# Optimization experiments

Measured on AMD Instinct MI355X. Metric: run time of the kernel, lower is better.

Reference implementation:

```python
import jax, jax.numpy as jnp
import numpy as np

N_NODES = 100000
N_EDGES = 1600000
IN_F, HID, OUT_F = 256, 128, 64
GAMMA = 1.0

def _glorot(key, shape):
    lim = (6.0 / (shape[0] + shape[1])) ** 0.5
    return jax.random.uniform(key, shape, jnp.float32, -lim, lim)

def setup_inputs() -> dict:
    key = jax.random.key(0)
    ks = jax.random.split(key, 8)
    x = jax.random.normal(ks[0], (N_NODES, IN_F), jnp.float32)
    src = jax.random.randint(ks[1], (N_EDGES,), 0, N_NODES)
    dst = jax.random.randint(ks[2], (N_EDGES,), 0, N_NODES)
    return dict(
        x=x, src=src, dst=dst,
        w_mean1=_glorot(ks[3], (IN_F, HID)), w_var1=_glorot(ks[4], (IN_F, HID)),
        b_mean1=jnp.zeros((HID,), jnp.float32), b_var1=jnp.zeros((HID,), jnp.float32),
        w_mean2=_glorot(ks[5], (HID, OUT_F)), w_var2=_glorot(ks[6], (HID, OUT_F)),
        b_mean2=jnp.zeros((OUT_F,), jnp.float32), b_var2=jnp.zeros((OUT_F,), jnp.float32),
    )

def _conv(mean_in, var_in, wm, wv, bm, bv, src, dst, norm1, norm2, gamma, act):
    n = norm1.shape[0]
    mean = jax.nn.relu(mean_in @ wm + bm)
    var = jax.nn.relu(var_in @ wv + bv)
    att = jnp.exp(-gamma * var)            # attention reweighting
    m = mean * att * norm1                  # pre-scaled messages [N, d]
    v = var * (att * att) * norm2
    # copy_u + sum: gather at src, scatter-add at dst
    mean = jax.ops.segment_sum(m[src], dst, num_segments=n) * norm1
    var = jax.ops.segment_sum(v[src], dst, num_segments=n) * norm2
    if act:
        mean, var = jax.nn.relu(mean), jax.nn.relu(var)
    return mean, var

def reference(x, src, dst, w_mean1, w_var1, b_mean1, b_var1,
              w_mean2, w_var2, b_mean2, b_var2):
    n = x.shape[0]
    ones = jnp.ones(dst.shape, jnp.float32)
    degs = jnp.clip(jax.ops.segment_sum(ones, dst, num_segments=n), 1.0, None)
    norm1 = (degs ** -0.5)[:, None]  # D^{-1/2}
    norm2 = norm1 * norm1            # D^{-1}
    # dropout is identity (eval mode) for a deterministic reference
    mean, var = _conv(x, x, w_mean1, w_var1, b_mean1, b_var1,
                      src, dst, norm1, norm2, GAMMA, True)
    mean, var = _conv(mean, var, w_mean2, w_var2, b_mean2, b_var2,
                      src, dst, norm1, norm2, GAMMA, False)
    std = jnp.sqrt(var + 1e-8)
    eps = jax.random.normal(jax.random.key(42), std.shape, std.dtype)
    return eps * std + mean
```

## Files before the change

kernel.cpp:

```cpp
#include <hip/hip_runtime.h>

#define GN 100000
#define GE 1600000

__device__ __forceinline__ unsigned bf16r(float f) {
  unsigned u = __float_as_uint(f);
  return (u + 0x7FFFu + ((u >> 16) & 1u)) >> 16;
}
__device__ __forceinline__ unsigned pack2(float lo, float hi) {
  return bf16r(lo) | (bf16r(hi) << 16);
}
__device__ __forceinline__ float bflo(unsigned u) { return __uint_as_float(u << 16); }
__device__ __forceinline__ float bfhi(unsigned u) { return __uint_as_float(u & 0xFFFF0000u); }

__device__ __forceinline__ unsigned rotl32(unsigned x, int r) { return (x << r) | (x >> (32 - r)); }

__device__ __forceinline__ void threefry2x32(unsigned k0, unsigned k1,
                                             unsigned c0, unsigned c1,
                                             unsigned& o0, unsigned& o1) {
  const unsigned ks2 = k0 ^ k1 ^ 0x1BD11BDAu;
  unsigned x0 = c0 + k0, x1 = c1 + k1;
#define TF_R4(ra, rb, rc, rd) \
  x0 += x1; x1 = rotl32(x1, ra); x1 ^= x0; \
  x0 += x1; x1 = rotl32(x1, rb); x1 ^= x0; \
  x0 += x1; x1 = rotl32(x1, rc); x1 ^= x0; \
  x0 += x1; x1 = rotl32(x1, rd); x1 ^= x0;
  TF_R4(13, 15, 26, 6)  x0 += k1;  x1 += ks2 + 1u;
  TF_R4(17, 29, 16, 24) x0 += ks2; x1 += k0 + 2u;
  TF_R4(13, 15, 26, 6)  x0 += k0;  x1 += k1 + 3u;
  TF_R4(17, 29, 16, 24) x0 += k1;  x1 += ks2 + 4u;
  TF_R4(13, 15, 26, 6)  x0 += ks2; x1 += k0 + 5u;
#undef TF_R4
  o0 = x0; o1 = x1;
}

__device__ __forceinline__ float bits_to_normal(unsigned bits) {
  const float lo = -0.99999994f;
  const float u = __uint_as_float((bits >> 9) | 0x3f800000u) - 1.0f;
  float x = u * 2.0f + lo;
  x = fmaxf(x, lo);
  float w = -log1pf(-x * x);
  float p;
  if (w < 5.0f) {
    w -= 2.5f;
    p = 2.81022636e-08f;
    p = fmaf(p, w, 3.43273939e-07f);
    p = fmaf(p, w, -3.5233877e-06f);
    p = fmaf(p, w, -4.39150654e-06f);
    p = fmaf(p, w, 0.00021858087f);
    p = fmaf(p, w, -0.00125372503f);
    p = fmaf(p, w, -0.00417768164f);
    p = fmaf(p, w, 0.246640727f);
    p = fmaf(p, w, 1.50140941f);
  } else {
    w = sqrtf(w) - 3.0f;
    p = -0.000200214257f;
    p = fmaf(p, w, 0.000100950558f);
    p = fmaf(p, w, 0.00134934322f);
    p = fmaf(p, w, -0.00367342844f);
    p = fmaf(p, w, 0.00573950773f);
    p = fmaf(p, w, -0.0076224613f);
    p = fmaf(p, w, 0.00943887047f);
    p = fmaf(p, w, 1.00167406f);
    p = fmaf(p, w, 2.83297682f);
  }
  return 1.41421356f * p * x;
}

__global__ void hist_kernel(const int* __restrict__ dst, int* __restrict__ hist) {
  const int e = blockIdx.x * 256 + threadIdx.x;
  if (e < GE) atomicAdd(&hist[dst[e]], 1);
}

__global__ __launch_bounds__(1024) void scan_kernel(const int* __restrict__ hist,
                                                    int* __restrict__ row_ptr) {
  __shared__ int wsum[16];
  __shared__ int carry_s;
  const int t = threadIdx.x, lane = t & 63, wave = t >> 6;
  if (t == 0) carry_s = 0;
  __syncthreads();
  for (int base = 0; base < GN; base += 4096) {
    const int idx = base + t * 4;
    const int h0 = (idx + 0 < GN) ? hist[idx + 0] : 0;
    const int h1 = (idx + 1 < GN) ? hist[idx + 1] : 0;
    const int h2 = (idx + 2 < GN) ? hist[idx + 2] : 0;
    const int h3 = (idx + 3 < GN) ? hist[idx + 3] : 0;
    const int p0 = h0, p1 = h0 + h1, p2 = h0 + h1 + h2, p3 = h0 + h1 + h2 + h3;
    int s = p3;
#pragma unroll
    for (int o = 1; o < 64; o <<= 1) {
      const int u = __shfl_up(s, o, 64);
      if (lane >= o) s += u;
    }
    if (lane == 63) wsum[wave] = s;
    __syncthreads();
    int woff = 0;
    for (int w2 = 0; w2 < wave; w2++) woff += wsum[w2];
    const int carry = carry_s;
    __syncthreads();
    const int tb = carry + woff + (s - p3);
    if (idx + 0 < GN) row_ptr[idx + 0] = tb;
    if (idx + 1 < GN) row_ptr[idx + 1] = tb + p0;
    if (idx + 2 < GN) row_ptr[idx + 2] = tb + p1;
    if (idx + 3 < GN) row_ptr[idx + 3] = tb + p2;
    if (t == 1023) carry_s = carry + woff + s;
    __syncthreads();
  }
  if (t == 0) row_ptr[GN] = carry_s;
}

__global__ void norm_kernel(const int* __restrict__ hist,
                            float* __restrict__ norm1, float* __restrict__ norm2) {
  const int i = blockIdx.x * 256 + threadIdx.x;
  if (i < GN) {
    const double d = (double)max(hist[i], 1);
    norm1[i] = (float)(1.0 / sqrt(d));
    norm2[i] = (float)(1.0 / d);
  }
}

__global__ void fill_kernel(const int* __restrict__ src, const int* __restrict__ dst,
                            const int* __restrict__ row_ptr, int* __restrict__ fillc,
                            int* __restrict__ csr) {
  const int e = blockIdx.x * 256 + threadIdx.x;
  if (e < GE) {
    const int d = dst[e];
    const int pos = atomicAdd(&fillc[d], 1);
    csr[row_ptr[d] + pos] = src[e];
  }
}

#define FMA8(acc, a, p0, p1)                                                        \
  acc[0] = fmaf(a, p0.x, acc[0]); acc[1] = fmaf(a, p0.y, acc[1]);                   \
  acc[2] = fmaf(a, p0.z, acc[2]); acc[3] = fmaf(a, p0.w, acc[3]);                   \
  acc[4] = fmaf(a, p1.x, acc[4]); acc[5] = fmaf(a, p1.y, acc[5]);                   \
  acc[6] = fmaf(a, p1.z, acc[6]); acc[7] = fmaf(a, p1.w, acc[7]);

__global__ __launch_bounds__(256) void gemm1_kernel(
    const float* __restrict__ x,
    const float* __restrict__ wm, const float* __restrict__ wv,
    const float* __restrict__ bm, const float* __restrict__ bv,
    const float* __restrict__ norm1, const float* __restrict__ norm2,
    unsigned* __restrict__ mv16) {
  __shared__ float xs[64][33];
  __shared__ float wms[32][128];
  __shared__ float wvs[32][128];
  const int t = threadIdx.x;
  const int row0 = blockIdx.x * 64;
  const int ty = t >> 4, tx = t & 15;
  float accm[4][8] = {};
  float accv[4][8] = {};
  for (int k0 = 0; k0 < 256; k0 += 32) {
#pragma unroll
    for (int i = 0; i < 2; i++) {
      const int f = t + (i << 8);
      const int r = f >> 3, c4 = (f & 7) << 2;
      const int rg = min(row0 + r, GN - 1);
      *(float4*)&xs[r][c4] = *(const float4*)&x[(size_t)rg * 256 + k0 + c4];
    }
#pragma unroll
    for (int i = 0; i < 4; i++) {
      const int f = t + (i << 8);
      const int kk = f >> 5, j4 = (f & 31) << 2;
      *(float4*)&wms[kk][j4] = *(const float4*)&wm[(size_t)(k0 + kk) * 128 + j4];
      *(float4*)&wvs[kk][j4] = *(const float4*)&wv[(size_t)(k0 + kk) * 128 + j4];
    }
    __syncthreads();
#pragma unroll 4
    for (int kk = 0; kk < 32; kk++) {
      const float4 bm0 = *(const float4*)&wms[kk][tx * 4];
      const float4 bm1 = *(const float4*)&wms[kk][tx * 4 + 64];
      const float4 bv0 = *(const float4*)&wvs[kk][tx * 4];
      const float4 bv1 = *(const float4*)&wvs[kk][tx * 4 + 64];
#pragma unroll
      for (int r = 0; r < 4; r++) {
        const float a = xs[ty * 4 + r][kk];
        FMA8(accm[r], a, bm0, bm1)
        FMA8(accv[r], a, bv0, bv1)
      }
    }
    __syncthreads();
  }
  float bmv[8], bvv[8];
#pragma unroll
  for (int j = 0; j < 4; j++) {
    bmv[j] = bm[tx * 4 + j];      bmv[4 + j] = bm[tx * 4 + 64 + j];
    bvv[j] = bv[tx * 4 + j];      bvv[4 + j] = bv[tx * 4 + 64 + j];
  }
#pragma unroll
  for (int rr = 0; rr < 4; rr++) {
    const int i = row0 + ty * 4 + rr;
    if (i >= GN) break;
    const float n1 = norm1[i], n2 = norm2[i];
    float om[8], ov[8];
#pragma unroll
    for (int j = 0; j < 8; j++) {
      const float mean = fmaxf(accm[rr][j] + bmv[j], 0.f);
      const float var  = fmaxf(accv[rr][j] + bvv[j], 0.f);
      const float att = expf(-var);
      om[j] = mean * att * n1;
      ov[j] = var * att * att * n2;
    }
    *(uint4*)(mv16 + (size_t)i * 128 + tx * 4) =
        make_uint4(pack2(om[0], om[1]), pack2(ov[0], ov[1]),
                   pack2(om[2], om[3]), pack2(ov[2], ov[3]));
    *(uint4*)(mv16 + (size_t)i * 128 + 64 + tx * 4) =
        make_uint4(pack2(om[4], om[5]), pack2(ov[4], ov[5]),
                   pack2(om[6], om[7]), pack2(ov[6], ov[7]));
  }
}

__global__ __launch_bounds__(256) void agg1_kernel(
    const int* __restrict__ row_ptr, const int* __restrict__ csr,
    const uint2* __restrict__ mv16,
    const float* __restrict__ norm1, const float* __restrict__ norm2,
    float* __restrict__ hmv) {
  const int wave = threadIdx.x >> 6, lane = threadIdx.x & 63;
  const int i = blockIdx.x * 4 + wave;
  const int e0 = row_ptr[i], e1 = row_ptr[i + 1];
  float amx0 = 0.f, amy0 = 0.f, avx0 = 0.f, avy0 = 0.f;
  float amx1 = 0.f, amy1 = 0.f, avx1 = 0.f, avy1 = 0.f;
  int e = e0;
  for (; e + 4 <= e1; e += 4) {
    const int s0 = csr[e], s1 = csr[e + 1], s2 = csr[e + 2], s3 = csr[e + 3];
    const uint2 q0 = mv16[(size_t)s0 * 64 + lane];
    const uint2 q1 = mv16[(size_t)s1 * 64 + lane];
    const uint2 q2 = mv16[(size_t)s2 * 64 + lane];
    const uint2 q3 = mv16[(size_t)s3 * 64 + lane];
    amx0 += bflo(q0.x) + bflo(q1.x); amx1 += bflo(q2.x) + bflo(q3.x);
    amy0 += bfhi(q0.x) + bfhi(q1.x); amy1 += bfhi(q2.x) + bfhi(q3.x);
    avx0 += bflo(q0.y) + bflo(q1.y); avx1 += bflo(q2.y) + bflo(q3.y);
    avy0 += bfhi(q0.y) + bfhi(q1.y); avy1 += bfhi(q2.y) + bfhi(q3.y);
  }
  for (; e < e1; e++) {
    const uint2 q0 = mv16[(size_t)csr[e] * 64 + lane];
    amx0 += bflo(q0.x); amy0 += bfhi(q0.x);
    avx0 += bflo(q0.y); avy0 += bfhi(q0.y);
  }
  const float amx = amx0 + amx1, amy = amy0 + amy1;
  const float avx = avx0 + avx1, avy = avy0 + avy1;
  const float n1 = norm1[i], n2 = norm2[i];
  float4 o;
  o.x = fmaxf(amx * n1, 0.f);
  o.y = fmaxf(avx * n2, 0.f);
  o.z = fmaxf(amy * n1, 0.f);
  o.w = fmaxf(avy * n2, 0.f);
  *(float4*)&hmv[(size_t)i * 256 + lane * 4] = o;
}

__global__ __launch_bounds__(256) void gemm2_kernel(
    const float* __restrict__ hmv,
    const float* __restrict__ wm2, const float* __restrict__ wv2,
    const float* __restrict__ bm2, const float* __restrict__ bv2,
    const float* __restrict__ norm1, const float* __restrict__ norm2,
    unsigned* __restrict__ m2v16) {
  __shared__ float wsh[2][64][64];
  const int t = threadIdx.x;
  const int r = t >> 3, c0 = (t & 7) << 3;
  const int i = blockIdx.x * 32 + r;
  const float* hrow = hmv + (size_t)i * 256;
  float accm[8] = {}, accv[8] = {};
  for (int kc = 0; kc < 2; kc++) {
#pragma unroll
    for (int ii = 0; ii < 4; ii++) {
      const int f4 = t + (ii << 8);
      const int k = f4 >> 4, j4 = (f4 & 15) << 2;
      *(float4*)&wsh[0][k][j4] = *(const float4*)&wm2[(size_t)(kc * 64 + k) * 64 + j4];
      *(float4*)&wsh[1][k][j4] = *(const float4*)&wv2[(size_t)(kc * 64 + k) * 64 + j4];
    }
    __syncthreads();
#pragma unroll 8
    for (int kk = 0; kk < 64; kk++) {
      const float2 hh = *(const float2*)&hrow[(kc * 64 + kk) * 2];
      const float4 b0 = *(const float4*)&wsh[0][kk][c0];
      const float4 b1 = *(const float4*)&wsh[0][kk][c0 + 4];
      const float4 d0 = *(const float4*)&wsh[1][kk][c0];
      const float4 d1 = *(const float4*)&wsh[1][kk][c0 + 4];
      FMA8(accm, hh.x, b0, b1)
      FMA8(accv, hh.y, d0, d1)
    }
    __syncthreads();
  }
  const float n1 = norm1[i], n2 = norm2[i];
  unsigned pk[8];
#pragma unroll
  for (int j = 0; j < 8; j++) {
    const float mean2 = fmaxf(accm[j] + bm2[c0 + j], 0.f);
    const float var2  = fmaxf(accv[j] + bv2[c0 + j], 0.f);
    const float att = expf(-var2);
    pk[j] = pack2(mean2 * att * n1, var2 * att * att * n2);
  }
  unsigned* dstp = m2v16 + (size_t)i * 64 + c0;
  *(uint4*)(dstp)     = make_uint4(pk[0], pk[1], pk[2], pk[3]);
  *(uint4*)(dstp + 4) = make_uint4(pk[4], pk[5], pk[6], pk[7]);
}

__global__ __launch_bounds__(256) void agg2_reparam_kernel(
    const int* __restrict__ row_ptr, const int* __restrict__ csr,
    const unsigned* __restrict__ m2v16,
    const float* __restrict__ norm1, const float* __restrict__ norm2,
    float* __restrict__ out) {
  const int wave = threadIdx.x >> 6, lane = threadIdx.x & 63;
  const int i = blockIdx.x * 4 + wave;
  const int e0 = row_ptr[i], e1 = row_ptr[i + 1];
  float am0 = 0.f, av0 = 0.f, am1 = 0.f, av1 = 0.f;
  int e = e0;
  for (; e + 4 <= e1; e += 4) {
    const int s0 = csr[e], s1 = csr[e + 1], s2 = csr[e + 2], s3 = csr[e + 3];
    const unsigned q0 = m2v16[(size_t)s0 * 64 + lane];
    const unsigned q1 = m2v16[(size_t)s1 * 64 + lane];
    const unsigned q2 = m2v16[(size_t)s2 * 64 + lane];
    const unsigned q3 = m2v16[(size_t)s3 * 64 + lane];
    am0 += bflo(q0) + bflo(q1); am1 += bflo(q2) + bflo(q3);
    av0 += bfhi(q0) + bfhi(q1); av1 += bfhi(q2) + bfhi(q3);
  }
  for (; e < e1; e++) {
    const unsigned q0 = m2v16[(size_t)csr[e] * 64 + lane];
    am0 += bflo(q0); av0 += bfhi(q0);
  }
  const float mean = (am0 + am1) * norm1[i];
  const float var  = (av0 + av1) * norm2[i];
  const int b = i * 64 + lane;
  unsigned o0, o1;
  threefry2x32(0u, 42u, 0u, (unsigned)b, o0, o1);
  const float eps = bits_to_normal(o0 ^ o1);
  out[b] = eps * sqrtf(var + 1e-8f) + mean;
}

extern "C" void kernel_launch(void* const* d_in, const int* in_sizes, int n_in,
                              void* d_out, int out_size, void* d_ws, size_t ws_size,
                              hipStream_t stream) {
  (void)in_sizes; (void)n_in; (void)out_size; (void)ws_size;
  const float* x   = (const float*)d_in[0];
  const int*   src = (const int*)d_in[1];
  const int*   dst = (const int*)d_in[2];
  const float* wm1 = (const float*)d_in[3];
  const float* wv1 = (const float*)d_in[4];
  const float* bm1 = (const float*)d_in[5];
  const float* bv1 = (const float*)d_in[6];
  const float* wm2 = (const float*)d_in[7];
  const float* wv2 = (const float*)d_in[8];
  const float* bm2 = (const float*)d_in[9];
  const float* bv2 = (const float*)d_in[10];
  float* out = (float*)d_out;

  char* base = (char*)d_ws;
  size_t off = 0;
  auto alloc = [&](size_t bytes) -> void* {
    void* p = base + off;
    off += (bytes + 255) & ~(size_t)255;
    return p;
  };
  int*      hist    = (int*)alloc((size_t)GN * 4);
  int*      row_ptr = (int*)alloc((size_t)(GN + 1) * 4);
  int*      fillc   = (int*)alloc((size_t)GN * 4);
  int*      csr     = (int*)alloc((size_t)GE * 4);
  float*    norm1   = (float*)alloc((size_t)GN * 4);
  float*    norm2   = (float*)alloc((size_t)GN * 4);
  unsigned* mv16    = (unsigned*)alloc((size_t)GN * 128 * 4);
  float*    hmv     = (float*)alloc((size_t)GN * 256 * 4);
  unsigned* m2v16   = mv16;

  hipMemsetAsync(hist, 0, (size_t)GN * 4, stream);
  hipMemsetAsync(fillc, 0, (size_t)GN * 4, stream);

  hist_kernel<<<(GE + 255) / 256, 256, 0, stream>>>(dst, hist);
  scan_kernel<<<1, 1024, 0, stream>>>(hist, row_ptr);
  norm_kernel<<<(GN + 255) / 256, 256, 0, stream>>>(hist, norm1, norm2);
  fill_kernel<<<(GE + 255) / 256, 256, 0, stream>>>(src, dst, row_ptr, fillc, csr);
  gemm1_kernel<<<(GN + 63) / 64, 256, 0, stream>>>(x, wm1, wv1, bm1, bv1, norm1, norm2, mv16);
  agg1_kernel<<<GN / 4, 256, 0, stream>>>(row_ptr, csr, (const uint2*)mv16, norm1, norm2, hmv);
  gemm2_kernel<<<GN / 32, 256, 0, stream>>>(hmv, wm2, wv2, bm2, bv2, norm1, norm2, m2v16);
  agg2_reparam_kernel<<<GN / 4, 256, 0, stream>>>(row_ptr, csr, m2v16, norm1, norm2, out);
}
```

Measured before the change: 781.7 us.

## Use fp16 MFMA for both GEMMs with prepacked weights and fp16 hidden features

Replaces the FP32 shared-memory SIMT GEMMs in both layers with 16x16x32 fp16 MFMA instructions. Weights are pre-packed into MFMA fragment layout by a new kernel. The first aggregation now writes the hidden mean and variance as packed fp16 into separate arrays, which halves intermediate traffic. Epilogues stage results through LDS so global stores are coalesced. The trade is lower input precision (x and weights cast to fp16) and one extra small launch.

Measured after the change: 658.6 us. 1.19x faster.

```diff
diff --git a/kernel.cpp b/kernel.cpp
--- a/kernel.cpp
+++ b/kernel.cpp
@@ -2,6 +2,11 @@
 
 #define GN 100000
 #define GE 1600000
+#define NT1 6250
+
+typedef _Float16 f16;
+typedef f16 f16x8 __attribute__((ext_vector_type(8)));
+typedef float f32x4 __attribute__((ext_vector_type(4)));
 
 __device__ __forceinline__ unsigned bf16r(float f) {
   unsigned u = __float_as_uint(f);
@@ -12,6 +17,12 @@
 }
 __device__ __forceinline__ float bflo(unsigned u) { return __uint_as_float(u << 16); }
 __device__ __forceinline__ float bfhi(unsigned u) { return __uint_as_float(u & 0xFFFF0000u); }
+
+__device__ __forceinline__ unsigned packf16(float a, float b) {
+  const unsigned ua = (unsigned)__builtin_bit_cast(unsigned short, (f16)a);
+  const unsigned ub = (unsigned)__builtin_bit_cast(unsigned short, (f16)b);
+  return ua | (ub << 16);
+}
 
 __device__ __forceinline__ unsigned rotl32(unsigned x, int r) { return (x << r) | (x >> (32 - r)); }
 
@@ -130,96 +141,93 @@
   }
 }
 
-#define FMA8(acc, a, p0, p1)                                                        \
-  acc[0] = fmaf(a, p0.x, acc[0]); acc[1] = fmaf(a, p0.y, acc[1]);                   \
-  acc[2] = fmaf(a, p0.z, acc[2]); acc[3] = fmaf(a, p0.w, acc[3]);                   \
-  acc[4] = fmaf(a, p1.x, acc[4]); acc[5] = fmaf(a, p1.y, acc[5]);                   \
-  acc[6] = fmaf(a, p1.z, acc[6]); acc[7] = fmaf(a, p1.w, acc[7]);
+__global__ __launch_bounds__(64) void pack_w_kernel(
+    const float* __restrict__ w1m, const float* __restrict__ w1v,
+    const float* __restrict__ w2m, const float* __restrict__ w2v,
+    f16* __restrict__ p1m, f16* __restrict__ p1v,
+    f16* __restrict__ p2m, f16* __restrict__ p2v) {
+  const int b = blockIdx.x, l = threadIdx.x;
+  const float* srcw; f16* dstw; int kt, nt, N;
+  if (b < 64)       { srcw = w1m; dstw = p1m; kt = b >> 3;         nt = b & 7;         N = 128; }
+  else if (b < 128) { srcw = w1v; dstw = p1v; kt = (b - 64) >> 3;  nt = (b - 64) & 7;  N = 128; }
+  else if (b < 144) { srcw = w2m; dstw = p2m; kt = (b - 128) >> 2; nt = (b - 128) & 3; N = 64; }
+  else              { srcw = w2v; dstw = p2v; kt = (b - 144) >> 2; nt = (b - 144) & 3; N = 64; }
+  const int NTn = N >> 4;
+  f16* out = dstw + ((size_t)(kt * NTn + nt) * 64 + l) * 8;
+  const int k0 = kt * 32 + (l >> 4) * 8;
+  const int c  = nt * 16 + (l & 15);
+#pragma unroll
+  for (int j = 0; j < 8; j++) out[j] = (f16)srcw[(size_t)(k0 + j) * N + c];
+}
 
 __global__ __launch_bounds__(256) void gemm1_kernel(
     const float* __restrict__ x,
-    const float* __restrict__ wm, const float* __restrict__ wv,
+    const f16x8* __restrict__ p1m, const f16x8* __restrict__ p1v,
     const float* __restrict__ bm, const float* __restrict__ bv,
     const float* __restrict__ norm1, const float* __restrict__ norm2,
     unsigned* __restrict__ mv16) {
-  __shared__ float xs[64][33];
-  __shared__ float wms[32][128];
-  __shared__ float wvs[32][128];
-  const int t = threadIdx.x;
-  const int row0 = blockIdx.x * 64;
-  const int ty = t >> 4, tx = t & 15;
-  float accm[4][8] = {};
-  float accv[4][8] = {};
-  for (int k0 = 0; k0 < 256; k0 += 32) {
-#pragma unroll
-    for (int i = 0; i < 2; i++) {
-      const int f = t + (i << 8);
-      const int r = f >> 3, c4 = (f & 7) << 2;
-      const int rg = min(row0 + r, GN - 1);
-      *(float4*)&xs[r][c4] = *(const float4*)&x[(size_t)rg * 256 + k0 + c4];
-    }
-#pragma unroll
-    for (int i = 0; i < 4; i++) {
-      const int f = t + (i << 8);
-      const int kk = f >> 5, j4 = (f & 31) << 2;
-      *(float4*)&wms[kk][j4] = *(const float4*)&wm[(size_t)(k0 + kk) * 128 + j4];
-      *(float4*)&wvs[kk][j4] = *(const float4*)&wv[(size_t)(k0 + kk) * 128 + j4];
-    }
-    __syncthreads();
-#pragma unroll 4
-    for (int kk = 0; kk < 32; kk++) {
-      const float4 bm0 = *(const float4*)&wms[kk][tx * 4];
-      const float4 bm1 = *(const float4*)&wms[kk][tx * 4 + 64];
-      const float4 bv0 = *(const float4*)&wvs[kk][tx * 4];
-      const float4 bv1 = *(const float4*)&wvs[kk][tx * 4 + 64];
-#pragma unroll
-      for (int r = 0; r < 4; r++) {
-        const float a = xs[ty * 4 + r][kk];
-        FMA8(accm[r], a, bm0, bm1)
-        FMA8(accv[r], a, bv0, bv1)
-      }
-    }
-    __syncthreads();
-  }
-  float bmv[8], bvv[8];
-#pragma unroll
-  for (int j = 0; j < 4; j++) {
-    bmv[j] = bm[tx * 4 + j];      bmv[4 + j] = bm[tx * 4 + 64 + j];
-    bvv[j] = bv[tx * 4 + j];      bvv[4 + j] = bv[tx * 4 + 64 + j];
-  }
-#pragma unroll
-  for (int rr = 0; rr < 4; rr++) {
-    const int i = row0 + ty * 4 + rr;
-    if (i >= GN) break;
-    const float n1 = norm1[i], n2 = norm2[i];
-    float om[8], ov[8];
-#pragma unroll
-    for (int j = 0; j < 8; j++) {
-      const float mean = fmaxf(accm[rr][j] + bmv[j], 0.f);
-      const float var  = fmaxf(accv[rr][j] + bvv[j], 0.f);
+  __shared__ unsigned ep[4][16][132];
+  const int wv = threadIdx.x >> 6, l = threadIdx.x & 63;
+  const int rt = blockIdx.x * 4 + wv;
+  if (rt >= NT1) return;
+  const int r0 = rt * 16;
+  const int lm = l & 15, lk = l >> 4;
+  f32x4 accm[8], accv[8];
+#pragma unroll
+  for (int nt = 0; nt < 8; nt++) {
+    accm[nt] = (f32x4){0.f, 0.f, 0.f, 0.f};
+    accv[nt] = (f32x4){0.f, 0.f, 0.f, 0.f};
+  }
+  const float* xrow = x + (size_t)(r0 + lm) * 256 + lk * 8;
+  for (int kt = 0; kt < 8; kt++) {
+    const float4 xlo = *(const float4*)(xrow + kt * 32);
+    const float4 xhi = *(const float4*)(xrow + kt * 32 + 4);
+    f16x8 a;
+    a[0] = (f16)xlo.x; a[1] = (f16)xlo.y; a[2] = (f16)xlo.z; a[3] = (f16)xlo.w;
+    a[4] = (f16)xhi.x; a[5] = (f16)xhi.y; a[6] = (f16)xhi.z; a[7] = (f16)xhi.w;
+#pragma unroll
+    for (int nt = 0; nt < 8; nt++) {
+      const f16x8 bmf = p1m[(kt * 8 + nt) * 64 + l];
+      const f16x8 bvf = p1v[(kt * 8 + nt) * 64 + l];
+      accm[nt] = __builtin_amdgcn_mfma_f32_16x16x32_f16(a, bmf, accm[nt], 0, 0, 0);
+      accv[nt] = __builtin_amdgcn_mfma_f32_16x16x32_f16(a, bvf, accv[nt], 0, 0, 0);
+    }
+  }
+  float n1r[4], n2r[4];
+#pragma unroll
+  for (int r = 0; r < 4; r++) {
+    n1r[r] = norm1[r0 + lk * 4 + r];
+    n2r[r] = norm2[r0 + lk * 4 + r];
+  }
+#pragma unroll
+  for (int nt = 0; nt < 8; nt++) {
+    const float bmc = bm[nt * 16 + lm];
+    const float bvc = bv[nt * 16 + lm];
+#pragma unroll
+    for (int r = 0; r < 4; r++) {
+      const float mean = fmaxf(accm[nt][r] + bmc, 0.f);
+      const float var  = fmaxf(accv[nt][r] + bvc, 0.f);
       const float att = expf(-var);
-      om[j] = mean * att * n1;
-      ov[j] = var * att * att * n2;
-    }
-    *(uint4*)(mv16 + (size_t)i * 128 + tx * 4) =
-        make_uint4(pack2(om[0], om[1]), pack2(ov[0], ov[1]),
-                   pack2(om[2], om[3]), pack2(ov[2], ov[3]));
-    *(uint4*)(mv16 + (size_t)i * 128 + 64 + tx * 4) =
-        make_uint4(pack2(om[4], om[5]), pack2(ov[4], ov[5]),
-                   pack2(om[6], om[7]), pack2(ov[6], ov[7]));
-  }
+      ep[wv][lk * 4 + r][nt * 16 + lm] = pack2(mean * att * n1r[r], var * att * att * n2r[r]);
+    }
+  }
+  asm volatile("s_waitcnt lgkmcnt(0)" ::: "memory");
+  unsigned* dstp = mv16 + (size_t)(r0 + lm) * 128 + lk * 32;
+#pragma unroll
+  for (int k2 = 0; k2 < 8; k2++)
+    *(uint4*)(dstp + k2 * 4) = *(uint4*)&ep[wv][lm][lk * 32 + k2 * 4];
 }
 
 __global__ __launch_bounds__(256) void agg1_kernel(
     const int* __restrict__ row_ptr, const int* __restrict__ csr,
     const uint2* __restrict__ mv16,
     const float* __restrict__ norm1, const float* __restrict__ norm2,
-    float* __restrict__ hmv) {
+    unsigned* __restrict__ hm, unsigned* __restrict__ hv) {
   const int wave = threadIdx.x >> 6, lane = threadIdx.x & 63;
   const int i = blockIdx.x * 4 + wave;
   const int e0 = row_ptr[i], e1 = row_ptr[i + 1];
-  float amx0 = 0.f, amy0 = 0.f, avx0 = 0.f, avy0 = 0.f;
-  float amx1 = 0.f, amy1 = 0.f, avx1 = 0.f, avy1 = 0.f;
+  float m0a = 0.f, m0b = 0.f, m1a = 0.f, m1b = 0.f;
+  float v0a = 0.f, v0b = 0.f, v1a = 0.f, v1b = 0.f;
   int e = e0;
   for (; e + 4 <= e1; e += 4) {
     const int s0 = csr[e], s1 = csr[e + 1], s2 = csr[e + 2], s3 = csr[e + 3];
@@ -227,72 +235,79 @@
     const uint2 q1 = mv16[(size_t)s1 * 64 + lane];
     const uint2 q2 = mv16[(size_t)s2 * 64 + lane];
     const uint2 q3 = mv16[(size_t)s3 * 64 + lane];
-    amx0 += bflo(q0.x) + bflo(q1.x); amx1 += bflo(q2.x) + bflo(q3.x);
-    amy0 += bfhi(q0.x) + bfhi(q1.x); amy1 += bfhi(q2.x) + bfhi(q3.x);
-    avx0 += bflo(q0.y) + bflo(q1.y); avx1 += bflo(q2.y) + bflo(q3.y);
-    avy0 += bfhi(q0.y) + bfhi(q1.y); avy1 += bfhi(q2.y) + bfhi(q3.y);
+    m0a += bflo(q0.x) + bflo(q1.x); m0b += bflo(q2.x) + bflo(q3.x);
+    v0a += bfhi(q0.x) + bfhi(q1.x); v0b += bfhi(q2.x) + bfhi(q3.x);
+    m1a += bflo(q0.y) + bflo(q1.y); m1b += bflo(q2.y) + bflo(q3.y);
+    v1a += bfhi(q0.y) + bfhi(q1.y); v1b += bfhi(q2.y) + bfhi(q3.y);
   }
   for (; e < e1; e++) {
     const uint2 q0 = mv16[(size_t)csr[e] * 64 + lane];
-    amx0 += bflo(q0.x); amy0 += bfhi(q0.x);
-    avx0 += bflo(q0.y); avy0 += bfhi(q0.y);
-  }
-  const float amx = amx0 + amx1, amy = amy0 + amy1;
-  const float avx = avx0 + avx1, avy = avy0 + avy1;
+    m0a += bflo(q0.x); v0a += bfhi(q0.x);
+    m1a += bflo(q0.y); v1a += bfhi(q0.y);
+  }
   const float n1 = norm1[i], n2 = norm2[i];
-  float4 o;
-  o.x = fmaxf(amx * n1, 0.f);
-  o.y = fmaxf(avx * n2, 0.f);
-  o.z = fmaxf(amy * n1, 0.f);
-  o.w = fmaxf(avy * n2, 0.f);
-  *(float4*)&hmv[(size_t)i * 256 + lane * 4] = o;
+  const float h_m0 = fmaxf((m0a + m0b) * n1, 0.f);
+  const float h_m1 = fmaxf((m1a + m1b) * n1, 0.f);
+  const float h_v0 = fmaxf((v0a + v0b) * n2, 0.f);
+  const float h_v1 = fmaxf((v1a + v1b) * n2, 0.f);
+  hm[(size_t)i * 64 + lane] = packf16(h_m0, h_m1);
+  hv[(size_t)i * 64 + lane] = packf16(h_v0, h_v1);
 }
 
 __global__ __launch_bounds__(256) void gemm2_kernel(
-    const float* __restrict__ hmv,
-    const float* __restrict__ wm2, const float* __restrict__ wv2,
+    const unsigned* __restrict__ hm, const unsigned* __restrict__ hv,
+    const f16x8* __restrict__ p2m, const f16x8* __restrict__ p2v,
     const float* __restrict__ bm2, const float* __restrict__ bv2,
     const float* __restrict__ norm1, const float* __restrict__ norm2,
     unsigned* __restrict__ m2v16) {
-  __shared__ float wsh[2][64][64];
-  const int t = threadIdx.x;
-  const int r = t >> 3, c0 = (t & 7) << 3;
-  const int i = blockIdx.x * 32 + r;
-  const float* hrow = hmv + (size_t)i * 256;
-  float accm[8] = {}, accv[8] = {};
-  for (int kc = 0; kc < 2; kc++) {
-#pragma unroll
-    for (int ii = 0; ii < 4; ii++) {
-      const int f4 = t + (ii << 8);
-      const int k = f4 >> 4, j4 = (f4 & 15) << 2;
-      *(float4*)&wsh[0][k][j4] = *(const float4*)&wm2[(size_t)(kc * 64 + k) * 64 + j4];
-      *(float4*)&wsh[1][k][j4] = *(const float4*)&wv2[(size_t)(kc * 64 + k) * 64 + j4];
-    }
-    __syncthreads();
-#pragma unroll 8
-    for (int kk = 0; kk < 64; kk++) {
-      const float2 hh = *(const float2*)&hrow[(kc * 64 + kk) * 2];
-      const float4 b0 = *(const float4*)&wsh[0][kk][c0];
-      const float4 b1 = *(const float4*)&wsh[0][kk][c0 + 4];
-      const float4 d0 = *(const float4*)&wsh[1][kk][c0];
-      const float4 d1 = *(const float4*)&wsh[1][kk][c0 + 4];
-      FMA8(accm, hh.x, b0, b1)
-      FMA8(accv, hh.y, d0, d1)
-    }
-    __syncthreads();
-  }
-  const float n1 = norm1[i], n2 = norm2[i];
-  unsigned pk[8];
-#pragma unroll
-  for (int j = 0; j < 8; j++) {
-    const float mean2 = fmaxf(accm[j] + bm2[c0 + j], 0.f);
-    const float var2  = fmaxf(accv[j] + bv2[c0 + j], 0.f);
-    const float att = expf(-var2);
-    pk[j] = pack2(mean2 * att * n1, var2 * att * att * n2);
-  }
-  unsigned* dstp = m2v16 + (size_t)i * 64 + c0;
-  *(uint4*)(dstp)     = make_uint4(pk[0], pk[1], pk[2], pk[3]);
-  *(uint4*)(dstp + 4) = make_uint4(pk[4], pk[5], pk[6], pk[7]);
+  __shared__ unsigned ep[4][16][68];
+  const int wv = threadIdx.x >> 6, l = threadIdx.x & 63;
+  const int rt = blockIdx.x * 4 + wv;
+  if (rt >= NT1) return;
+  const int r0 = rt * 16;
+  const int lm = l & 15, lk = l >> 4;
+  f32x4 accm[4], accv[4];
+#pragma unroll
+  for (int nt = 0; nt < 4; nt++) {
+    accm[nt] = (f32x4){0.f, 0.f, 0.f, 0.f};
+    accv[nt] = (f32x4){0.f, 0.f, 0.f, 0.f};
+  }
+  const f16x8* hmrow = (const f16x8*)(hm + (size_t)(r0 + lm) * 64);
+  const f16x8* hvrow = (const f16x8*)(hv + (size_t)(r0 + lm) * 64);
+  for (int kt = 0; kt < 4; kt++) {
+    const f16x8 am = hmrow[kt * 4 + lk];
+    const f16x8 av = hvrow[kt * 4 + lk];
+#pragma unroll
+    for (int nt = 0; nt < 4; nt++) {
+      const f16x8 bmf = p2m[(kt * 4 + nt) * 64 + l];
+      const f16x8 bvf = p2v[(kt * 4 + nt) * 64 + l];
+      accm[nt] = __builtin_amdgcn_mfma_f32_16x16x32_f16(am, bmf, accm[nt], 0, 0, 0);
+      accv[nt] = __builtin_amdgcn_mfma_f32_16x16x32_f16(av, bvf, accv[nt], 0, 0, 0);
+    }
+  }
+  float n1r[4], n2r[4];
+#pragma unroll
+  for (int r = 0; r < 4; r++) {
+    n1r[r] = norm1[r0 + lk * 4 + r];
+    n2r[r] = norm2[r0 + lk * 4 + r];
+  }
+#pragma unroll
+  for (int nt = 0; nt < 4; nt++) {
+    const float bmc = bm2[nt * 16 + lm];
+    const float bvc = bv2[nt * 16 + lm];
+#pragma unroll
+    for (int r = 0; r < 4; r++) {
+      const float mean2 = fmaxf(accm[nt][r] + bmc, 0.f);
+      const float var2  = fmaxf(accv[nt][r] + bvc, 0.f);
+      const float att = expf(-var2);
+      ep[wv][lk * 4 + r][nt * 16 + lm] = pack2(mean2 * att * n1r[r], var2 * att * att * n2r[r]);
+    }
+  }
+  asm volatile("s_waitcnt lgkmcnt(0)" ::: "memory");
+  unsigned* dstp = m2v16 + (size_t)(r0 + lm) * 64 + lk * 16;
+#pragma unroll
+  for (int k2 = 0; k2 < 4; k2++)
+    *(uint4*)(dstp + k2 * 4) = *(uint4*)&ep[wv][lm][lk * 16 + k2 * 4];
 }
 
 __global__ __launch_bounds__(256) void agg2_reparam_kernel(
@@ -358,18 +373,26 @@
   float*    norm1   = (float*)alloc((size_t)GN * 4);
   float*    norm2   = (float*)alloc((size_t)GN * 4);
   unsigned* mv16    = (unsigned*)alloc((size_t)GN * 128 * 4);
-  float*    hmv     = (float*)alloc((size_t)GN * 256 * 4);
+  unsigned* hm      = (unsigned*)alloc((size_t)GN * 64 * 4);
+  unsigned* hv      = (unsigned*)alloc((size_t)GN * 64 * 4);
+  f16*      p1m     = (f16*)alloc((size_t)256 * 128 * 2);
+  f16*      p1v     = (f16*)alloc((size_t)256 * 128 * 2);
+  f16*      p2m     = (f16*)alloc((size_t)128 * 64 * 2);
+  f16*      p2v     = (f16*)alloc((size_t)128 * 64 * 2);
   unsigned* m2v16   = mv16;
 
   hipMemsetAsync(hist, 0, (size_t)GN * 4, stream);
   hipMemsetAsync(fillc, 0, (size_t)GN * 4, stream);
 
+  pack_w_kernel<<<160, 64, 0, stream>>>(wm1, wv1, wm2, wv2, p1m, p1v, p2m, p2v);
   hist_kernel<<<(GE + 255) / 256, 256, 0, stream>>>(dst, hist);
   scan_kernel<<<1, 1024, 0, stream>>>(hist, row_ptr);
   norm_kernel<<<(GN + 255) / 256, 256, 0, stream>>>(hist, norm1, norm2);
   fill_kernel<<<(GE + 255) / 256, 256, 0, stream>>>(src, dst, row_ptr, fillc, csr);
-  gemm1_kernel<<<(GN + 63) / 64, 256, 0, stream>>>(x, wm1, wv1, bm1, bv1, norm1, norm2, mv16);
-  agg1_kernel<<<GN / 4, 256, 0, stream>>>(row_ptr, csr, (const uint2*)mv16, norm1, norm2, hmv);
-  gemm2_kernel<<<GN / 32, 256, 0, stream>>>(hmv, wm2, wv2, bm2, bv2, norm1, norm2, m2v16);
+  gemm1_kernel<<<(NT1 + 3) / 4, 256, 0, stream>>>(x, (const f16x8*)p1m, (const f16x8*)p1v,
+                                                  bm1, bv1, norm1, norm2, mv16);
+  agg1_kernel<<<GN / 4, 256, 0, stream>>>(row_ptr, csr, (const uint2*)mv16, norm1, norm2, hm, hv);
+  gemm2_kernel<<<(NT1 + 3) / 4, 256, 0, stream>>>(hm, hv, (const f16x8*)p2m, (const f16x8*)p2v,
+                                                  bm2, bv2, norm1, norm2, m2v16);
   agg2_reparam_kernel<<<GN / 4, 256, 0, stream>>>(row_ptr, csr, m2v16, norm1, norm2, out);
 }
```
